# Kernel tuning notes

Measured on AMD Instinct MI355X. Metric: run time of the kernel, lower is better.

Reference implementation:

```python
import jax, jax.numpy as jnp
import numpy as np

N, E, EU, L2, EL, G = 50000, 800000, 400000, 131072, 1048576, 512
ND, ED, H, NH, NL, OUT = 128, 16, 128, 4, 2, 1
HD = H // NH


def _ln(x, g, b):
    m = x.mean(-1, keepdims=True)
    v = ((x - m) ** 2).mean(-1, keepdims=True)
    return (x - m) * jax.lax.rsqrt(v + 1e-5) * g + b


def _gcn(x, w, b, ei, n):
    # GCNConv: add self-loops, symmetric normalization, aggregate at ei[1]
    xw = x @ w.T
    loop = jnp.arange(n)
    src = jnp.concatenate([ei[0], loop])
    dst = jnp.concatenate([ei[1], loop])
    deg = jax.ops.segment_sum(jnp.ones_like(src, x.dtype), dst, n)
    dinv = jnp.where(deg > 0, jax.lax.rsqrt(deg), 0.0)
    norm = (dinv[src] * dinv[dst])[:, None]
    return jax.ops.segment_sum(norm * xw[src], dst, n) + b


def _mha(xs, in_w, in_b, out_w, out_b):
    B, S, _ = xs.shape
    qkv = xs @ in_w.T + in_b                       # [B,S,3H]
    q, k, v = jnp.split(qkv, 3, axis=-1)
    hd = lambda a: a.reshape(B, S, NH, HD).transpose(0, 2, 1, 3)
    q, k, v = hd(q), hd(k), hd(v)
    att = jax.nn.softmax(jnp.einsum('bhqd,bhkd->bhqk', q, k) / jnp.sqrt(jnp.float32(HD)), axis=-1)
    o = jnp.einsum('bhqk,bhkd->bhqd', att, v).transpose(0, 2, 1, 3).reshape(B, S, H)
    return o @ out_w.T + out_b


def _encoder(xs, p):
    # torch TransformerEncoderLayer, post-norm, relu activation, dropout=0 (eval)
    for i in range(NL):
        a = _mha(xs, p['in_w'][i], p['in_b'][i], p['out_w'][i], p['out_b'][i])
        xs = _ln(xs + a, p['ln1_g'][i], p['ln1_b'][i])
        ff = jax.nn.relu(xs @ p['ff1_w'][i].T + p['ff1_b'][i]) @ p['ff2_w'][i].T + p['ff2_b'][i]
        xs = _ln(xs + ff, p['ln2_g'][i], p['ln2_b'][i])
    return xs


def _multi_pool(x, idx, g):
    cnt = jax.ops.segment_sum(jnp.ones((x.shape[0],), x.dtype), idx, g)
    mean = jax.ops.segment_sum(x, idx, g) / jnp.maximum(cnt, 1.0)[:, None]
    mx = jax.ops.segment_max(x, idx, g)
    mn = jax.ops.segment_min(x, idx, g)
    mx = jnp.where(jnp.isfinite(mx), mx, 0.0)
    mn = jnp.where(jnp.isfinite(mn), mn, 0.0)
    return jnp.concatenate([mn, mx, mean], axis=-1)


def setup_inputs() -> dict:
    key = jax.random.key(0)
    ks = jax.random.split(key, 40)
    r = lambda i, shape: jax.random.normal(ks[i], shape, jnp.float32) * 0.02
    inp = {}
    inp['x'] = jax.random.normal(ks[0], (N, ND), jnp.float32)
    inp['edge_attr'] = jax.random.normal(ks[1], (EU, ED), jnp.float32)
    inp['edge_index'] = jax.random.randint(ks[2], (2, E), 0, N)
    inp['unique_edges'] = jax.random.randint(ks[3], (2, EU), 0, N)
    inp['batch'] = jnp.sort(jax.random.randint(ks[4], (N,), 0, G))
    inp['l2_node_mapping'] = jax.random.randint(ks[5], (2, L2), 0, EU)
    inp['l2_edge_index'] = jax.random.randint(ks[6], (2, EL), 0, L2)
    inp['num_graphs'] = G
    inp['lin_edge_w'] = r(7, (H, ED)); inp['lin_edge_b'] = jnp.zeros((H,))
    inp['gcn1_w'] = r(8, (H, ND)); inp['gcn1_b'] = jnp.zeros((H,))
    inp['gcn2_w'] = r(9, (H, H)); inp['gcn2_b'] = jnp.zeros((H,))
    inp['t_in_w'] = r(10, (NL, 3 * H, H)); inp['t_in_b'] = jnp.zeros((NL, 3 * H))
    inp['t_out_w'] = r(11, (NL, H, H)); inp['t_out_b'] = jnp.zeros((NL, H))
    inp['t_ln1_g'] = jnp.ones((NL, H)); inp['t_ln1_b'] = jnp.zeros((NL, H))
    inp['t_ln2_g'] = jnp.ones((NL, H)); inp['t_ln2_b'] = jnp.zeros((NL, H))
    inp['t_ff1_w'] = r(12, (NL, 2 * H, H)); inp['t_ff1_b'] = jnp.zeros((NL, 2 * H))
    inp['t_ff2_w'] = r(13, (NL, H, 2 * H)); inp['t_ff2_b'] = jnp.zeros((NL, H))
    inp['f0_w'] = r(14, (H, 9 * H)); inp['f0_b'] = jnp.zeros((H,))
    inp['f0_g'] = jnp.ones((H,)); inp['f0_beta'] = jnp.zeros((H,))
    inp['f1_w'] = r(15, (H, H)); inp['f1_b'] = jnp.zeros((H,))
    inp['f1_g'] = jnp.ones((H,)); inp['f1_beta'] = jnp.zeros((H,))
    inp['fo_w'] = r(16, (OUT, H)); inp['fo_b'] = jnp.zeros((OUT,))
    return inp


def reference(x, edge_attr, lin_edge_w, lin_edge_b, gcn1_w, gcn1_b, gcn2_w, gcn2_b,
              t_in_w, t_in_b, t_out_w, t_out_b, t_ln1_g, t_ln1_b, t_ln2_g, t_ln2_b,
              t_ff1_w, t_ff1_b, t_ff2_w, t_ff2_b, f0_w, f0_b, f0_g, f0_beta,
              f1_w, f1_b, f1_g, f1_beta, fo_w, fo_b,
              edge_index, unique_edges, batch, l2_node_mapping, l2_edge_index, num_graphs):
    H0_edge = edge_attr @ lin_edge_w.T + lin_edge_b                 # [EU,H]
    H0 = _gcn(x, gcn1_w, gcn1_b, edge_index, x.shape[0])            # [N,H]
    e_idx, f_idx = l2_node_mapping[0], l2_node_mapping[1]
    u, v = unique_edges[0, e_idx], unique_edges[1, e_idx]
    s, t = unique_edges[0, f_idx], unique_edges[1, f_idx]
    H0_set = jnp.stack([H0[u], H0[v], H0[s], H0[t], H0_edge[e_idx], H0_edge[f_idx]], axis=1)  # [L2,6,H]
    tp = dict(in_w=t_in_w, in_b=t_in_b, out_w=t_out_w, out_b=t_out_b,
              ln1_g=t_ln1_g, ln1_b=t_ln1_b, ln2_g=t_ln2_g, ln2_b=t_ln2_b,
              ff1_w=t_ff1_w, ff1_b=t_ff1_b, ff2_w=t_ff2_w, ff2_b=t_ff2_b)
    H1 = _encoder(H0_set, tp).mean(axis=1)                          # [L2,H]
    l2_batch = batch[u]
    H2 = jax.nn.relu(_gcn(H1, gcn2_w, gcn2_b, l2_edge_index, H1.shape[0]))
    H0_pool = _multi_pool(H0, batch, num_graphs)
    H1_pool = _multi_pool(H1, l2_batch, num_graphs)
    H2_pool = _multi_pool(H2, l2_batch, num_graphs)
    Hp = jnp.concatenate([H0_pool, H1_pool, H2_pool], axis=1)       # [G,9H]
    h = jax.nn.gelu(_ln(Hp @ f0_w.T + f0_b, f0_g, f0_beta), approximate=False)
    h = jax.nn.gelu(_ln(h @ f1_w.T + f1_b, f1_g, f1_beta), approximate=False)
    return h @ fo_w.T + fo_b
```

## Files before the change

### kernel.cpp

```cpp
#include <hip/hip_runtime.h>

constexpr int cN  = 50000;
constexpr int cE  = 800000;
constexpr int cEU = 400000;
constexpr int cL2 = 131072;
constexpr int cEL = 1048576;
constexpr int cG  = 512;
constexpr int cH  = 128;
constexpr int cNH = 4;
constexpr int cNL = 2;

constexpr int CAP1 = 64;
constexpr int CAP2 = 48;

constexpr int ESETS = 8;
constexpr int ERT   = ESETS * 6;
constexpr int MT    = 3;
constexpr int QS    = 388;
constexpr int AS    = 264;

constexpr int OFF_QKV = 0;
constexpr int OFF_AH  = 74496;
constexpr int OFF_AL  = OFF_AH + 25344;
constexpr int OFF_ATT = OFF_AL + 25344;
constexpr int OFF_IDX = OFF_ATT + 4608;
constexpr int SMEM_SZ = OFF_IDX + 192;

typedef __attribute__((ext_vector_type(8))) short short8v;
typedef __attribute__((ext_vector_type(4))) float f32x4;

#define DEVI __device__ __forceinline__

DEVI unsigned fmap(float x) {
  unsigned u = __float_as_uint(x);
  return (u & 0x80000000u) ? ~u : (u | 0x80000000u);
}
DEVI float funmap(unsigned m) {
  return __uint_as_float((m & 0x80000000u) ? (m & 0x7FFFFFFFu) : ~m);
}
DEVI float gelu_exact(float x) {
  return 0.5f * x * (1.0f + erff(x * 0.70710678118654752f));
}
DEVI unsigned short f2b_rn(float x) {
  unsigned u = __float_as_uint(x);
  return (unsigned short)((u + 0x7FFFu + ((u >> 16) & 1u)) >> 16);
}
DEVI float b2f(unsigned short h) { return __uint_as_float(((unsigned)h) << 16); }
DEVI void sp2(unsigned short* hi, unsigned short* lo, int idx, float a0, float a1) {
  unsigned short h0 = f2b_rn(a0), h1 = f2b_rn(a1);
  unsigned short l0 = f2b_rn(a0 - b2f(h0)), l1 = f2b_rn(a1 - b2f(h1));
  *(unsigned*)&hi[idx] = (unsigned)h0 | ((unsigned)h1 << 16);
  *(unsigned*)&lo[idx] = (unsigned)l0 | ((unsigned)l1 << 16);
}
DEVI void sp4(unsigned short* hi, unsigned short* lo, int idx, float4 v) {
  unsigned short h0 = f2b_rn(v.x), h1 = f2b_rn(v.y), h2 = f2b_rn(v.z), h3 = f2b_rn(v.w);
  unsigned short l0 = f2b_rn(v.x - b2f(h0)), l1 = f2b_rn(v.y - b2f(h1));
  unsigned short l2 = f2b_rn(v.z - b2f(h2)), l3 = f2b_rn(v.w - b2f(h3));
  uint2 H, L;
  H.x = (unsigned)h0 | ((unsigned)h1 << 16);
  H.y = (unsigned)h2 | ((unsigned)h3 << 16);
  L.x = (unsigned)l0 | ((unsigned)l1 << 16);
  L.y = (unsigned)l2 | ((unsigned)l3 << 16);
  *(uint2*)&hi[idx] = H;
  *(uint2*)&lo[idx] = L;
}

__global__ void fill_k(float* p, float v, int n) {
  int i = blockIdx.x * 256 + threadIdx.x;
  if (i < n) p[i] = v;
}

__global__ void deg_count_k(const int* __restrict__ ei, float* deg, int nE) {
  int e = blockIdx.x * 256 + threadIdx.x;
  if (e < nE) atomicAdd(&deg[ei[nE + e]], 1.0f);
}

__global__ void to_dinv_k(float* deg, int n) {
  int i = blockIdx.x * 256 + threadIdx.x;
  if (i < n) deg[i] = rsqrtf(deg[i]);
}

__global__ void csr_fill_k(const int* __restrict__ ei, int* __restrict__ cnt,
                           int* __restrict__ csr, int cap, int nE) {
  int e = blockIdx.x * 256 + threadIdx.x;
  if (e >= nE) return;
  int s = ei[e], d = ei[nE + e];
  int slot = atomicAdd(&cnt[d], 1);
  if (slot < cap) csr[(long)d * cap + slot] = s;
}

__global__ void split_w_k(const float* __restrict__ src, unsigned short* __restrict__ hi,
                          unsigned short* __restrict__ lo, int n) {
  int i = blockIdx.x * 256 + threadIdx.x;
  if (i < n) {
    float x = src[i];
    unsigned short h = f2b_rn(x);
    hi[i] = h;
    lo[i] = f2b_rn(x - b2f(h));
  }
}

__global__ __launch_bounds__(256) void gemm128_k(const float* __restrict__ A,
                                                 const float* __restrict__ W,
                                                 float* __restrict__ C, int M) {
  __shared__ float At[16][132];
  int c = threadIdx.x & 127, rr = threadIdx.x >> 7;
  int base = blockIdx.x * 128;
  for (int tile = 0; tile < 8; ++tile) {
    int r0 = base + tile * 16;
    if (r0 >= M) break;
    __syncthreads();
    for (int i = threadIdx.x; i < 16 * 32; i += 256) {
      int r = i >> 5, s4 = (i & 31) * 4;
      if (r0 + r < M) *(float4*)&At[r][s4] = *(const float4*)&A[(long)(r0 + r) * cH + s4];
    }
    __syncthreads();
    float acc[8];
    #pragma unroll
    for (int j = 0; j < 8; ++j) acc[j] = 0.f;
    const float* wr = W + (long)c * cH;
    for (int k = 0; k < cH; k += 4) {
      float4 w4 = *(const float4*)(wr + k);
      #pragma unroll
      for (int j = 0; j < 8; ++j) {
        float4 a4 = *(const float4*)&At[rr * 8 + j][k];
        acc[j] = fmaf(a4.x, w4.x, acc[j]);
        acc[j] = fmaf(a4.y, w4.y, acc[j]);
        acc[j] = fmaf(a4.z, w4.z, acc[j]);
        acc[j] = fmaf(a4.w, w4.w, acc[j]);
      }
    }
    #pragma unroll
    for (int j = 0; j < 8; ++j) {
      int r = r0 + rr * 8 + j;
      if (r < M) C[(long)r * cH + c] = acc[j];
    }
  }
}

template<int STORE>
__global__ __launch_bounds__(256) void gcn_gather_k(
    const float* __restrict__ xw, const float* __restrict__ dinv,
    const int* __restrict__ csr, const int* __restrict__ cnt,
    const float* __restrict__ bias, float* __restrict__ out,
    const int* __restrict__ gidx,
    float* __restrict__ sum, unsigned* __restrict__ mx, unsigned* __restrict__ mn,
    float* __restrict__ ccnt, int n, int cap) {
  int wv = threadIdx.x >> 6, lane = threadIdx.x & 63;
  int r = blockIdx.x * 4 + wv;
  if (r >= n) return;
  int c = lane * 2;
  float di = dinv[r];
  float2 v0 = *(const float2*)&xw[(long)r * cH + c];
  float2 b2 = *(const float2*)&bias[c];
  float a0 = b2.x + di * di * v0.x;
  float a1 = b2.y + di * di * v0.y;
  int deg = cnt[r];
  if (deg > cap) deg = cap;
  long base = (long)r * cap;
  for (int k = 0; k < deg; ++k) {
    int s = csr[base + k];
    float w = dinv[s] * di;
    float2 v = *(const float2*)&xw[(long)s * cH + c];
    a0 = fmaf(w, v.x, a0);
    a1 = fmaf(w, v.y, a1);
  }
  if (STORE) {
    float2 o; o.x = a0; o.y = a1;
    *(float2*)&out[(long)r * cH + c] = o;
  } else {
    a0 = fmaxf(a0, 0.f);
    a1 = fmaxf(a1, 0.f);
    int g = gidx[r];
    long b = (long)g * cH + c;
    atomicAdd(&sum[b + 0], a0); atomicAdd(&sum[b + 1], a1);
    atomicMax(&mx[b + 0], fmap(a0)); atomicMax(&mx[b + 1], fmap(a1));
    atomicMin(&mn[b + 0], fmap(a0)); atomicMin(&mn[b + 1], fmap(a1));
    if (lane == 0) atomicAdd(&ccnt[g], 1.0f);
  }
}

__global__ __launch_bounds__(512, 1) void encoder_k(
    const float* __restrict__ H0, const float* __restrict__ EA,
    const float* __restrict__ LEW, const float* __restrict__ LEB,
    const int* __restrict__ ue, const int* __restrict__ l2nm,
    const int* __restrict__ batch,
    const unsigned short* __restrict__ WinH, const unsigned short* __restrict__ WinL,
    const float* __restrict__ Bin,
    const unsigned short* __restrict__ WoutH, const unsigned short* __restrict__ WoutL,
    const float* __restrict__ Bout,
    const float* __restrict__ Ln1g, const float* __restrict__ Ln1b,
    const float* __restrict__ Ln2g, const float* __restrict__ Ln2b,
    const unsigned short* __restrict__ Wf1H, const unsigned short* __restrict__ Wf1L,
    const float* __restrict__ Bf1,
    const unsigned short* __restrict__ Wf2H, const unsigned short* __restrict__ Wf2L,
    const float* __restrict__ Bf2,
    float* __restrict__ H1,
    float* __restrict__ sum1, unsigned* __restrict__ mx1, unsigned* __restrict__ mn1,
    float* __restrict__ cnt1, int* __restrict__ l2b) {
  extern __shared__ char smem[];
  float* QKV = (float*)(smem + OFF_QKV);
  unsigned short* Ahs = (unsigned short*)(smem + OFF_AH);
  unsigned short* Als = (unsigned short*)(smem + OFF_AL);
  float* att = (float*)(smem + OFF_ATT);
  int* nidx = (int*)(smem + OFF_IDX);
  int* eidx = nidx + 32;

  const int tid = threadIdx.x;
  const int lane = tid & 63, wv = tid >> 6;
  const int lr = lane & 15, lq = lane >> 4;
  const int base = blockIdx.x * ESETS;

  if (tid < ESETS) {
    int e = l2nm[base + tid];
    int f = l2nm[cL2 + base + tid];
    eidx[tid * 2 + 0] = e;
    eidx[tid * 2 + 1] = f;
    nidx[tid * 4 + 0] = ue[e];
    nidx[tid * 4 + 1] = ue[cEU + e];
    nidx[tid * 4 + 2] = ue[f];
    nidx[tid * 4 + 3] = ue[cEU + f];
  }
  __syncthreads();
  for (int i = tid; i < 32 * 32; i += 512) {
    int q = i >> 5, s4 = (i & 31) * 4;
    int r = (q >> 2) * 6 + (q & 3);
    float4 v = *(const float4*)&H0[(long)nidx[q] * cH + s4];
    sp4(Ahs, Als, r * AS + s4, v);
  }
  for (int i = tid; i < ESETS * cH; i += 512) {
    int c = (i & 63) * 2, q = i >> 6;
    const float* row = EA + (long)eidx[q] * 16;
    const float* w0 = LEW + c * 16;
    const float* w1 = LEW + (c + 1) * 16;
    float2 bb2 = *(const float2*)&LEB[c];
    float a0 = bb2.x, a1 = bb2.y;
    #pragma unroll
    for (int d = 0; d < 16; ++d) {
      float rv = row[d];
      a0 = fmaf(rv, w0[d], a0);
      a1 = fmaf(rv, w1[d], a1);
    }
    int r = (q >> 1) * 6 + 4 + (q & 1);
    sp2(Ahs, Als, r * AS + c, a0, a1);
  }
  __syncthreads();

  for (int l = 0; l < cNL; ++l) {
    {
      const unsigned short* WH = WinH + (long)l * 384 * 128;
      const unsigned short* WL = WinL + (long)l * 384 * 128;
      const float* BB = Bin + l * 384;
      #pragma unroll
      for (int ni = 0; ni < 3; ++ni) {
        int col = (wv + 8 * ni) * 16 + lr;
        const unsigned short* wp = WH + (long)col * 128 + (lq << 3);
        const unsigned short* wq = WL + (long)col * 128 + (lq << 3);
        f32x4 accH[MT], accL1[MT], accL2[MT];
        #pragma unroll
        for (int m = 0; m < MT; ++m) {
          accH[m] = (f32x4){0.f, 0.f, 0.f, 0.f};
          accL1[m] = (f32x4){0.f, 0.f, 0.f, 0.f};
          accL2[m] = (f32x4){0.f, 0.f, 0.f, 0.f};
        }
        #pragma unroll
        for (int ks = 0; ks < 4; ++ks) {
          short8v bh = *(const short8v*)&wp[ks * 32];
          short8v bl = *(const short8v*)&wq[ks * 32];
          #pragma unroll
          for (int m = 0; m < MT; ++m) {
            int ao = (m * 16 + lr) * AS + (lq << 3) + ks * 32;
            short8v ah = *(const short8v*)&Ahs[ao];
            short8v al = *(const short8v*)&Als[ao];
            accL1[m] = __builtin_amdgcn_mfma_f32_16x16x32_bf16(al, bh, accL1[m], 0, 0, 0);
            accL2[m] = __builtin_amdgcn_mfma_f32_16x16x32_bf16(ah, bl, accL2[m], 0, 0, 0);
            accH[m] = __builtin_amdgcn_mfma_f32_16x16x32_bf16(ah, bh, accH[m], 0, 0, 0);
          }
        }
        float bv = BB[col];
        #pragma unroll
        for (int m = 0; m < MT; ++m) {
          int r0 = m * 16 + (lq << 2);
          #pragma unroll
          for (int j = 0; j < 4; ++j)
            QKV[(r0 + j) * QS + col] = accH[m][j] + (accL1[m][j] + accL2[m][j]) + bv;
        }
      }
    }
    __syncthreads();
    {
      const int s = wv;
      float* attS = att + s * 144;
      if (lane < 24) {
        int h = lane / 6, qt = lane % 6;
        const float* qp = &QKV[(s * 6 + qt) * QS + h * 32];
        float4 qv[8];
        #pragma unroll
        for (int j4 = 0; j4 < 8; ++j4) qv[j4] = *(const float4*)&qp[j4 * 4];
        float sc[6];
        #pragma unroll
        for (int kt = 0; kt < 6; ++kt) {
          const float* kp = &QKV[(s * 6 + kt) * QS + 128 + h * 32];
          float d = 0.f;
          #pragma unroll
          for (int j4 = 0; j4 < 8; ++j4) {
            float4 b4 = *(const float4*)&kp[j4 * 4];
            d = fmaf(qv[j4].x, b4.x, d); d = fmaf(qv[j4].y, b4.y, d);
            d = fmaf(qv[j4].z, b4.z, d); d = fmaf(qv[j4].w, b4.w, d);
          }
          sc[kt] = d * 0.17677669529663687f;
        }
        float mx = sc[0];
        #pragma unroll
        for (int kt = 1; kt < 6; ++kt) mx = fmaxf(mx, sc[kt]);
        float ev[6]; float sum = 0.f;
        #pragma unroll
        for (int kt = 0; kt < 6; ++kt) { ev[kt] = expf(sc[kt] - mx); sum += ev[kt]; }
        float inv = 1.f / sum;
        #pragma unroll
        for (int kt = 0; kt < 6; ++kt) attS[(h * 6 + qt) * 6 + kt] = ev[kt] * inv;
      }
      asm volatile("s_waitcnt lgkmcnt(0)" ::: "memory");
      __builtin_amdgcn_sched_barrier(0);
      {
        int c = lane * 2;
        int h = c >> 5;
        #pragma unroll
        for (int r = 0; r < 6; ++r) {
          const float* arow = &attS[(h * 6 + r) * 6];
          float d0 = 0.f, d1 = 0.f;
          #pragma unroll
          for (int kt = 0; kt < 6; ++kt) {
            float2 v2 = *(const float2*)&QKV[(s * 6 + kt) * QS + 256 + c];
            float a = arow[kt];
            d0 = fmaf(a, v2.x, d0);
            d1 = fmaf(a, v2.y, d1);
          }
          sp2(Ahs, Als, (s * 6 + r) * AS + 128 + c, d0, d1);
        }
      }
    }
    __syncthreads();
    {
      const unsigned short* WH = WoutH + (long)l * 128 * 128;
      const unsigned short* WL = WoutL + (long)l * 128 * 128;
      int col = wv * 16 + lr;
      const unsigned short* wp = WH + (long)col * 128 + (lq << 3);
      const unsigned short* wq = WL + (long)col * 128 + (lq << 3);
      f32x4 accH[MT], accL1[MT], accL2[MT];
      #pragma unroll
      for (int m = 0; m < MT; ++m) {
        accH[m] = (f32x4){0.f, 0.f, 0.f, 0.f};
        accL1[m] = (f32x4){0.f, 0.f, 0.f, 0.f};
        accL2[m] = (f32x4){0.f, 0.f, 0.f, 0.f};
      }
      #pragma unroll
      for (int ks = 0; ks < 4; ++ks) {
        short8v bh = *(const short8v*)&wp[ks * 32];
        short8v bl = *(const short8v*)&wq[ks * 32];
        #pragma unroll
        for (int m = 0; m < MT; ++m) {
          int ao = (m * 16 + lr) * AS + 128 + (lq << 3) + ks * 32;
          short8v ah = *(const short8v*)&Ahs[ao];
          short8v al = *(const short8v*)&Als[ao];
          accL1[m] = __builtin_amdgcn_mfma_f32_16x16x32_bf16(al, bh, accL1[m], 0, 0, 0);
          accL2[m] = __builtin_amdgcn_mfma_f32_16x16x32_bf16(ah, bl, accL2[m], 0, 0, 0);
          accH[m] = __builtin_amdgcn_mfma_f32_16x16x32_bf16(ah, bh, accH[m], 0, 0, 0);
        }
      }
      float bv = Bout[l * 128 + col];
      #pragma unroll
      for (int m = 0; m < MT; ++m) {
        int r0 = m * 16 + (lq << 2);
        #pragma unroll
        for (int j = 0; j < 4; ++j)
          QKV[(r0 + j) * QS + col] = accH[m][j] + (accL1[m][j] + accL2[m][j]) + bv;
      }
    }
    __syncthreads();
    {
      const float* gg = Ln1g + l * cH;
      const float* bb = Ln1b + l * cH;
      #pragma unroll
      for (int p = 0; p < MT; ++p) {
        int r = p * 16 + (tid >> 5);
        int c0 = (tid & 31) * 4;
        ushort4 ah4 = *(const ushort4*)&Ahs[r * AS + c0];
        ushort4 al4 = *(const ushort4*)&Als[r * AS + c0];
        float4 q4 = *(const float4*)&QKV[r * QS + c0];
        float y[4];
        y[0] = b2f(ah4.x) + b2f(al4.x) + q4.x;
        y[1] = b2f(ah4.y) + b2f(al4.y) + q4.y;
        y[2] = b2f(ah4.z) + b2f(al4.z) + q4.z;
        y[3] = b2f(ah4.w) + b2f(al4.w) + q4.w;
        float s = 0.f, s2 = 0.f;
        #pragma unroll
        for (int j = 0; j < 4; ++j) { s += y[j]; s2 += y[j] * y[j]; }
        #pragma unroll
        for (int m = 1; m < 32; m <<= 1) { s += __shfl_xor(s, m, 32); s2 += __shfl_xor(s2, m, 32); }
        float mean = s * (1.f / 128.f);
        float rstd = rsqrtf(s2 * (1.f / 128.f) - mean * mean + 1e-5f);
        float4 g4 = *(const float4*)&gg[c0];
        float4 b4v = *(const float4*)&bb[c0];
        float4 xn4;
        xn4.x = (y[0] - mean) * rstd * g4.x + b4v.x;
        xn4.y = (y[1] - mean) * rstd * g4.y + b4v.y;
        xn4.z = (y[2] - mean) * rstd * g4.z + b4v.z;
        xn4.w = (y[3] - mean) * rstd * g4.w + b4v.w;
        *(float4*)&QKV[r * QS + 128 + c0] = xn4;
        sp4(Ahs, Als, r * AS + c0, xn4);
      }
    }
    __syncthreads();
    {
      const unsigned short* WH = Wf1H + (long)l * 256 * 128;
      const unsigned short* WL = Wf1L + (long)l * 256 * 128;
      #pragma unroll
      for (int ni = 0; ni < 2; ++ni) {
        int col = (wv + 8 * ni) * 16 + lr;
        const unsigned short* wp = WH + (long)col * 128 + (lq << 3);
        const unsigned short* wq = WL + (long)col * 128 + (lq << 3);
        f32x4 accH[MT], accL1[MT], accL2[MT];
        #pragma unroll
        for (int m = 0; m < MT; ++m) {
          accH[m] = (f32x4){0.f, 0.f, 0.f, 0.f};
          accL1[m] = (f32x4){0.f, 0.f, 0.f, 0.f};
          accL2[m] = (f32x4){0.f, 0.f, 0.f, 0.f};
        }
        #pragma unroll
        for (int ks = 0; ks < 4; ++ks) {
          short8v bh = *(const short8v*)&wp[ks * 32];
          short8v bl = *(const short8v*)&wq[ks * 32];
          #pragma unroll
          for (int m = 0; m < MT; ++m) {
            int ao = (m * 16 + lr) * AS + (lq << 3) + ks * 32;
            short8v ah = *(const short8v*)&Ahs[ao];
            short8v al = *(const short8v*)&Als[ao];
            accL1[m] = __builtin_amdgcn_mfma_f32_16x16x32_bf16(al, bh, accL1[m], 0, 0, 0);
            accL2[m] = __builtin_amdgcn_mfma_f32_16x16x32_bf16(ah, bl, accL2[m], 0, 0, 0);
            accH[m] = __builtin_amdgcn_mfma_f32_16x16x32_bf16(ah, bh, accH[m], 0, 0, 0);
          }
        }
        int lc = col + (col >= 128 ? 128 : 0);
        #pragma unroll
        for (int m = 0; m < MT; ++m) {
          int r0 = m * 16 + (lq << 2);
          #pragma unroll
          for (int j = 0; j < 4; ++j)
            QKV[(r0 + j) * QS + lc] = accH[m][j] + (accL1[m][j] + accL2[m][j]);
        }
      }
    }
    __syncthreads();
    for (int i = tid; i < ERT * 128; i += 512) {
      int r = i >> 7, n = (i & 127) * 2;
      int lc = n + (n >= 128 ? 128 : 0);
      float2 v2 = *(const float2*)&QKV[r * QS + lc];
      float2 bb2 = *(const float2*)&Bf1[l * 256 + n];
      float h0 = fmaxf(v2.x + bb2.x, 0.f);
      float h1 = fmaxf(v2.y + bb2.y, 0.f);
      sp2(Ahs, Als, r * AS + n, h0, h1);
    }
    __syncthreads();
    {
      const unsigned short* WH = Wf2H + (long)l * 128 * 256;
      const unsigned short* WL = Wf2L + (long)l * 128 * 256;
      int col = wv * 16 + lr;
      const unsigned short* wp = WH + (long)col * 256 + (lq << 3);
      const unsigned short* wq = WL + (long)col * 256 + (lq << 3);
      f32x4 accH[MT], accL1[MT], accL2[MT];
      #pragma unroll
      for (int m = 0; m < MT; ++m) {
        accH[m] = (f32x4){0.f, 0.f, 0.f, 0.f};
        accL1[m] = (f32x4){0.f, 0.f, 0.f, 0.f};
        accL2[m] = (f32x4){0.f, 0.f, 0.f, 0.f};
      }
      #pragma unroll
      for (int ks = 0; ks < 8; ++ks) {
        short8v bh = *(const short8v*)&wp[ks * 32];
        short8v bl = *(const short8v*)&wq[ks * 32];
        #pragma unroll
        for (int m = 0; m < MT; ++m) {
          int ao = (m * 16 + lr) * AS + (lq << 3) + ks * 32;
          short8v ah = *(const short8v*)&Ahs[ao];
          short8v al = *(const short8v*)&Als[ao];
          accL1[m] = __builtin_amdgcn_mfma_f32_16x16x32_bf16(al, bh, accL1[m], 0, 0, 0);
          accL2[m] = __builtin_amdgcn_mfma_f32_16x16x32_bf16(ah, bl, accL2[m], 0, 0, 0);
          accH[m] = __builtin_amdgcn_mfma_f32_16x16x32_bf16(ah, bh, accH[m], 0, 0, 0);
        }
      }
      float bv = Bf2[l * 128 + col];
      #pragma unroll
      for (int m = 0; m < MT; ++m) {
        int r0 = m * 16 + (lq << 2);
        #pragma unroll
        for (int j = 0; j < 4; ++j)
          QKV[(r0 + j) * QS + col] = accH[m][j] + (accL1[m][j] + accL2[m][j]) + bv;
      }
    }
    __syncthreads();
    {
      const float* gg = Ln2g + l * cH;
      const float* bb = Ln2b + l * cH;
      #pragma unroll
      for (int p = 0; p < MT; ++p) {
        int r = p * 16 + (tid >> 5);
        int c0 = (tid & 31) * 4;
        float4 qa = *(const float4*)&QKV[r * QS + 128 + c0];
        float4 qb = *(const float4*)&QKV[r * QS + c0];
        float y[4];
        y[0] = qa.x + qb.x; y[1] = qa.y + qb.y;
        y[2] = qa.z + qb.z; y[3] = qa.w + qb.w;
        float s = 0.f, s2 = 0.f;
        #pragma unroll
        for (int j = 0; j < 4; ++j) { s += y[j]; s2 += y[j] * y[j]; }
        #pragma unroll
        for (int m = 1; m < 32; m <<= 1) { s += __shfl_xor(s, m, 32); s2 += __shfl_xor(s2, m, 32); }
        float mean = s * (1.f / 128.f);
        float rstd = rsqrtf(s2 * (1.f / 128.f) - mean * mean + 1e-5f);
        float4 g4 = *(const float4*)&gg[c0];
        float4 b4v = *(const float4*)&bb[c0];
        float4 xn4;
        xn4.x = (y[0] - mean) * rstd * g4.x + b4v.x;
        xn4.y = (y[1] - mean) * rstd * g4.y + b4v.y;
        xn4.z = (y[2] - mean) * rstd * g4.z + b4v.z;
        xn4.w = (y[3] - mean) * rstd * g4.w + b4v.w;
        sp4(Ahs, Als, r * AS + c0, xn4);
      }
    }
    __syncthreads();
  }

  {
    int s = tid >> 6, c = (tid & 63) * 2;
    float m0 = 0.f, m1 = 0.f;
    #pragma unroll
    for (int t = 0; t < 6; ++t) {
      unsigned hh = *(const unsigned*)&Ahs[(s * 6 + t) * AS + c];
      unsigned ll = *(const unsigned*)&Als[(s * 6 + t) * AS + c];
      m0 += b2f((unsigned short)(hh & 0xFFFFu)) + b2f((unsigned short)(ll & 0xFFFFu));
      m1 += b2f((unsigned short)(hh >> 16)) + b2f((unsigned short)(ll >> 16));
    }
    float v0 = m0 * (1.f / 6.f), v1 = m1 * (1.f / 6.f);
    float2 o; o.x = v0; o.y = v1;
    *(float2*)&H1[(long)(base + s) * cH + c] = o;
    int g = batch[nidx[s * 4]];
    long b = (long)g * cH + c;
    atomicAdd(&sum1[b + 0], v0);  atomicAdd(&sum1[b + 1], v1);
    atomicMax(&mx1[b + 0], fmap(v0)); atomicMax(&mx1[b + 1], fmap(v1));
    atomicMin(&mn1[b + 0], fmap(v0)); atomicMin(&mn1[b + 1], fmap(v1));
    if (c == 0) {
      atomicAdd(&cnt1[g], 1.0f);
      l2b[base + s] = g;
    }
  }
}

__global__ void init_stats3_k(char* ST, size_t stride) {
  int i = blockIdx.x * 256 + threadIdx.x;
  if (i >= cG * cH) return;
  #pragma unroll
  for (int p = 0; p < 3; ++p) {
    char* b = ST + (size_t)p * stride;
    ((float*)b)[i] = 0.f;
    ((unsigned*)(b + (size_t)cG * cH * 4))[i] = 0u;
    ((unsigned*)(b + (size_t)cG * cH * 8))[i] = 0xFFFFFFFFu;
    if (i < cG) ((float*)(b + (size_t)cG * cH * 12))[i] = 0.f;
  }
}

__global__ void pool_sorted_k(const float* __restrict__ X, const int* __restrict__ gidx,
                              float* sum, unsigned* mx, unsigned* mn, float* cnt, int n) {
  long t = (long)blockIdx.x * 256 + threadIdx.x;
  int q = (int)(t & 31) * 4;
  long r0 = (t >> 5) * 8;
  if (r0 >= n) return;
  int gcur = -1;
  float s0 = 0, s1 = 0, s2 = 0, s3 = 0, cc = 0;
  float x0 = 0, x1 = 0, x2 = 0, x3 = 0;
  float n0 = 0, n1 = 0, n2 = 0, n3 = 0;
  for (int k = 0; k < 8; ++k) {
    long r = r0 + k;
    if (r >= n) break;
    int g = gidx[r];
    float4 v = *(const float4*)&X[r * cH + q];
    if (g != gcur) {
      if (gcur >= 0) {
        long b = (long)gcur * cH + q;
        atomicAdd(&sum[b + 0], s0); atomicAdd(&sum[b + 1], s1);
        atomicAdd(&sum[b + 2], s2); atomicAdd(&sum[b + 3], s3);
        atomicMax(&mx[b + 0], fmap(x0)); atomicMax(&mx[b + 1], fmap(x1));
        atomicMax(&mx[b + 2], fmap(x2)); atomicMax(&mx[b + 3], fmap(x3));
        atomicMin(&mn[b + 0], fmap(n0)); atomicMin(&mn[b + 1], fmap(n1));
        atomicMin(&mn[b + 2], fmap(n2)); atomicMin(&mn[b + 3], fmap(n3));
        if (q == 0) atomicAdd(&cnt[gcur], cc);
      }
      gcur = g;
      s0 = v.x; s1 = v.y; s2 = v.z; s3 = v.w;
      x0 = v.x; x1 = v.y; x2 = v.z; x3 = v.w;
      n0 = v.x; n1 = v.y; n2 = v.z; n3 = v.w;
      cc = 1.f;
    } else {
      s0 += v.x; s1 += v.y; s2 += v.z; s3 += v.w;
      x0 = fmaxf(x0, v.x); x1 = fmaxf(x1, v.y); x2 = fmaxf(x2, v.z); x3 = fmaxf(x3, v.w);
      n0 = fminf(n0, v.x); n1 = fminf(n1, v.y); n2 = fminf(n2, v.z); n3 = fminf(n3, v.w);
      cc += 1.f;
    }
  }
  if (gcur >= 0) {
    long b = (long)gcur * cH + q;
    atomicAdd(&sum[b + 0], s0); atomicAdd(&sum[b + 1], s1);
    atomicAdd(&sum[b + 2], s2); atomicAdd(&sum[b + 3], s3);
    atomicMax(&mx[b + 0], fmap(x0)); atomicMax(&mx[b + 1], fmap(x1));
    atomicMax(&mx[b + 2], fmap(x2)); atomicMax(&mx[b + 3], fmap(x3));
    atomicMin(&mn[b + 0], fmap(n0)); atomicMin(&mn[b + 1], fmap(n1));
    atomicMin(&mn[b + 2], fmap(n2)); atomicMin(&mn[b + 3], fmap(n3));
    if (q == 0) atomicAdd(&cnt[gcur], cc);
  }
}

__global__ __launch_bounds__(128) void mlp_k(
    const char* __restrict__ ST, size_t stride,
    const float* __restrict__ f0w, const float* __restrict__ f0b,
    const float* __restrict__ f0g, const float* __restrict__ f0bb,
    const float* __restrict__ f1w, const float* __restrict__ f1b,
    const float* __restrict__ f1g, const float* __restrict__ f1bb,
    const float* __restrict__ fow, const float* __restrict__ fob,
    float* __restrict__ out) {
  __shared__ float hin[1152];
  __shared__ float red[8];
  int g = blockIdx.x, tid = threadIdx.x;
  #pragma unroll
  for (int p = 0; p < 3; ++p) {
    const char* b = ST + (size_t)p * stride;
    const float* sum = (const float*)b;
    const unsigned* mx = (const unsigned*)(b + (size_t)cG * cH * 4);
    const unsigned* mn = (const unsigned*)(b + (size_t)cG * cH * 8);
    const float* cnt = (const float*)(b + (size_t)cG * cH * 12);
    int idx = g * cH + tid;
    float ct = cnt[g];
    float mean = sum[idx] / fmaxf(ct, 1.f);
    float mxv = (ct > 0.f) ? funmap(mx[idx]) : 0.f;
    float mnv = (ct > 0.f) ? funmap(mn[idx]) : 0.f;
    hin[p * 384 + tid] = mnv;
    hin[p * 384 + 128 + tid] = mxv;
    hin[p * 384 + 256 + tid] = mean;
  }
  __syncthreads();
  float acc = f0b[tid];
  {
    const float* wr = f0w + (long)tid * 1152;
    for (int k = 0; k < 1152; k += 4) {
      float4 w4 = *(const float4*)(wr + k);
      float4 h4 = *(const float4*)&hin[k];
      acc = fmaf(h4.x, w4.x, acc);
      acc = fmaf(h4.y, w4.y, acc);
      acc = fmaf(h4.z, w4.z, acc);
      acc = fmaf(h4.w, w4.w, acc);
    }
  }
  float s = acc, s2 = acc * acc;
  #pragma unroll
  for (int m = 1; m < 64; m <<= 1) { s += __shfl_xor(s, m); s2 += __shfl_xor(s2, m); }
  if ((tid & 63) == 0) { red[tid >> 6] = s; red[4 + (tid >> 6)] = s2; }
  __syncthreads();
  s = red[0] + red[1]; s2 = red[4] + red[5];
  {
    float mean = s * (1.f / 128.f);
    float rstd = rsqrtf(s2 * (1.f / 128.f) - mean * mean + 1e-5f);
    float xn = (acc - mean) * rstd * f0g[tid] + f0bb[tid];
    float h0 = gelu_exact(xn);
    __syncthreads();
    hin[tid] = h0;
  }
  __syncthreads();
  acc = f1b[tid];
  {
    const float* wr = f1w + (long)tid * 128;
    for (int k = 0; k < 128; k += 4) {
      float4 w4 = *(const float4*)(wr + k);
      float4 h4 = *(const float4*)&hin[k];
      acc = fmaf(h4.x, w4.x, acc);
      acc = fmaf(h4.y, w4.y, acc);
      acc = fmaf(h4.z, w4.z, acc);
      acc = fmaf(h4.w, w4.w, acc);
    }
  }
  s = acc; s2 = acc * acc;
  #pragma unroll
  for (int m = 1; m < 64; m <<= 1) { s += __shfl_xor(s, m); s2 += __shfl_xor(s2, m); }
  __syncthreads();
  if ((tid & 63) == 0) { red[tid >> 6] = s; red[4 + (tid >> 6)] = s2; }
  __syncthreads();
  s = red[0] + red[1]; s2 = red[4] + red[5];
  float h1;
  {
    float mean = s * (1.f / 128.f);
    float rstd = rsqrtf(s2 * (1.f / 128.f) - mean * mean + 1e-5f);
    float xn = (acc - mean) * rstd * f1g[tid] + f1bb[tid];
    h1 = gelu_exact(xn);
  }
  float p = h1 * fow[tid];
  #pragma unroll
  for (int m = 1; m < 64; m <<= 1) p += __shfl_xor(p, m);
  __syncthreads();
  if ((tid & 63) == 0) red[tid >> 6] = p;
  __syncthreads();
  if (tid == 0) out[g] = red[0] + red[1] + fob[0];
}

extern "C" void kernel_launch(void* const* d_in, const int* in_sizes, int n_in,
                              void* d_out, int out_size, void* d_ws, size_t ws_size,
                              hipStream_t stream) {
  const float* x     = (const float*)d_in[0];
  const float* ea    = (const float*)d_in[1];
  const int*   ei    = (const int*)d_in[2];
  const int*   ue    = (const int*)d_in[3];
  const int*   batch = (const int*)d_in[4];
  const int*   l2nm  = (const int*)d_in[5];
  const int*   l2ei  = (const int*)d_in[6];
  const float* lew   = (const float*)d_in[8];
  const float* leb   = (const float*)d_in[9];
  const float* g1w   = (const float*)d_in[10];
  const float* g1b   = (const float*)d_in[11];
  const float* g2w   = (const float*)d_in[12];
  const float* g2b   = (const float*)d_in[13];
  const float* tinw  = (const float*)d_in[14];
  const float* tinb  = (const float*)d_in[15];
  const float* toutw = (const float*)d_in[16];
  const float* toutb = (const float*)d_in[17];
  const float* tl1g  = (const float*)d_in[18];
  const float* tl1b  = (const float*)d_in[19];
  const float* tl2g  = (const float*)d_in[20];
  const float* tl2b  = (const float*)d_in[21];
  const float* tf1w  = (const float*)d_in[22];
  const float* tf1b  = (const float*)d_in[23];
  const float* tf2w  = (const float*)d_in[24];
  const float* tf2b  = (const float*)d_in[25];
  const float* f0w   = (const float*)d_in[26];
  const float* f0b   = (const float*)d_in[27];
  const float* f0g   = (const float*)d_in[28];
  const float* f0bb  = (const float*)d_in[29];
  const float* f1w   = (const float*)d_in[30];
  const float* f1b   = (const float*)d_in[31];
  const float* f1g   = (const float*)d_in[32];
  const float* f1bb  = (const float*)d_in[33];
  const float* fow   = (const float*)d_in[34];
  const float* fob   = (const float*)d_in[35];
  float* out = (float*)d_out;

  char* ws = (char*)d_ws;
  size_t off = 0;
  float* H1  = (float*)(ws + off);  off += (size_t)cL2 * cH * 4;
  float* H0  = (float*)(ws + off);  off += (size_t)cL2 * cH * 4;
  float* XW  = (float*)(ws + off);  off += (size_t)cL2 * cH * 4;
  float* DEG = (float*)(ws + off);  off += (size_t)cL2 * 4;
  int*   L2B = (int*)(ws + off);    off += (size_t)cL2 * 4;
  int*   CNT = (int*)(ws + off);    off += (size_t)cL2 * 4;
  char*  ST  = ws + off;            off += 3 * ((size_t)cG * cH * 4 * 3 + cG * 4);
  int*   CSR1 = (int*)(ws + off);   off += (size_t)cN * CAP1 * 4;
  int*   CSR2 = (int*)(ws + off);   off += (size_t)cL2 * CAP2 * 4;
  unsigned short* WinH  = (unsigned short*)(ws + off); off += (size_t)cNL * 384 * 128 * 2;
  unsigned short* WinL  = (unsigned short*)(ws + off); off += (size_t)cNL * 384 * 128 * 2;
  unsigned short* WoutH = (unsigned short*)(ws + off); off += (size_t)cNL * 128 * 128 * 2;
  unsigned short* WoutL = (unsigned short*)(ws + off); off += (size_t)cNL * 128 * 128 * 2;
  unsigned short* Wf1H  = (unsigned short*)(ws + off); off += (size_t)cNL * 256 * 128 * 2;
  unsigned short* Wf1L  = (unsigned short*)(ws + off); off += (size_t)cNL * 256 * 128 * 2;
  unsigned short* Wf2H  = (unsigned short*)(ws + off); off += (size_t)cNL * 128 * 256 * 2;
  unsigned short* Wf2L  = (unsigned short*)(ws + off); off += (size_t)cNL * 128 * 256 * 2;

  size_t st_stride = (size_t)cG * cH * 4 * 3 + cG * 4;
  auto stat = [&](int p) {
    char* b = ST + p * st_stride;
    struct S { float* sum; unsigned* mx; unsigned* mn; float* cnt; } s;
    s.sum = (float*)b;
    s.mx  = (unsigned*)(b + (size_t)cG * cH * 4);
    s.mn  = (unsigned*)(b + (size_t)cG * cH * 8);
    s.cnt = (float*)(b + (size_t)cG * cH * 12);
    return s;
  };
  auto s0 = stat(0), s1 = stat(1), s2 = stat(2);

  split_w_k<<<(cNL * 384 * 128 + 255) / 256, 256, 0, stream>>>(tinw, WinH, WinL, cNL * 384 * 128);
  split_w_k<<<(cNL * 128 * 128 + 255) / 256, 256, 0, stream>>>(toutw, WoutH, WoutL, cNL * 128 * 128);
  split_w_k<<<(cNL * 256 * 128 + 255) / 256, 256, 0, stream>>>(tf1w, Wf1H, Wf1L, cNL * 256 * 128);
  split_w_k<<<(cNL * 128 * 256 + 255) / 256, 256, 0, stream>>>(tf2w, Wf2H, Wf2L, cNL * 128 * 256);
  init_stats3_k<<<(cG * cH + 255) / 256, 256, 0, stream>>>(ST, st_stride);

  gemm128_k<<<(cN + 127) / 128, 256, 0, stream>>>(x, g1w, XW, cN);
  fill_k<<<(cN + 255) / 256, 256, 0, stream>>>(DEG, 1.0f, cN);
  deg_count_k<<<(cE + 255) / 256, 256, 0, stream>>>(ei, DEG, cE);
  to_dinv_k<<<(cN + 255) / 256, 256, 0, stream>>>(DEG, cN);
  fill_k<<<(cN + 255) / 256, 256, 0, stream>>>((float*)CNT, 0.0f, cN);
  csr_fill_k<<<(cE + 255) / 256, 256, 0, stream>>>(ei, CNT, CSR1, CAP1, cE);
  gcn_gather_k<1><<<(cN + 3) / 4, 256, 0, stream>>>(XW, DEG, CSR1, CNT, g1b, H0,
      nullptr, nullptr, nullptr, nullptr, nullptr, cN, CAP1);

  hipFuncSetAttribute(reinterpret_cast<const void*>(encoder_k),
                      hipFuncAttributeMaxDynamicSharedMemorySize, 131072);
  encoder_k<<<cL2 / ESETS, 512, SMEM_SZ, stream>>>(H0, ea, lew, leb, ue, l2nm, batch,
      WinH, WinL, tinb, WoutH, WoutL, toutb, tl1g, tl1b, tl2g, tl2b,
      Wf1H, Wf1L, tf1b, Wf2H, Wf2L, tf2b, H1,
      s1.sum, s1.mx, s1.mn, s1.cnt, L2B);

  pool_sorted_k<<<(int)((((long)(cN + 7) / 8) * 32 + 255) / 256), 256, 0, stream>>>(
      H0, batch, s0.sum, s0.mx, s0.mn, s0.cnt, cN);

  gemm128_k<<<(cL2 + 127) / 128, 256, 0, stream>>>(H1, g2w, XW, cL2);
  fill_k<<<(cL2 + 255) / 256, 256, 0, stream>>>(DEG, 1.0f, cL2);
  deg_count_k<<<(cEL + 255) / 256, 256, 0, stream>>>(l2ei, DEG, cEL);
  to_dinv_k<<<(cL2 + 255) / 256, 256, 0, stream>>>(DEG, cL2);
  fill_k<<<(cL2 + 255) / 256, 256, 0, stream>>>((float*)CNT, 0.0f, cL2);
  csr_fill_k<<<(cEL + 255) / 256, 256, 0, stream>>>(l2ei, CNT, CSR2, CAP2, cEL);
  gcn_gather_k<0><<<(cL2 + 3) / 4, 256, 0, stream>>>(XW, DEG, CSR2, CNT, g2b, nullptr,
      L2B, s2.sum, s2.mx, s2.mn, s2.cnt, cL2, CAP2);

  mlp_k<<<cG, 128, 0, stream>>>(ST, st_stride, f0w, f0b, f0g, f0bb, f1w, f1b, f1g, f1bb, fow, fob, out);
}
```

Before: 4.360 ms.

## Shrink encoder tile to four sets for multi-block occupancy; derive degree from CSR counts

The encoder kernel now processes 4 edge-sets per block instead of 8, shrinking shared memory to about 73KB and raising launch bounds so several blocks can share a CU. The MFMA tile count drops to 2 with padded rows zeroed and guarded stores. The separate degree atomic pass is removed and inverse sqrt degree is computed from the CSR fill counts. The trade-off is more blocks with padding waste (24 of 32 rows used) and lower weight reuse per block. It also relies on the CSR counts being uncapped atomic counts.

```diff
diff --git a/kernel.cpp b/kernel.cpp
--- a/kernel.cpp
+++ b/kernel.cpp
@@ -13,18 +13,18 @@
 constexpr int CAP1 = 64;
 constexpr int CAP2 = 48;
 
-constexpr int ESETS = 8;
+constexpr int ESETS = 4;
 constexpr int ERT   = ESETS * 6;
-constexpr int MT    = 3;
+constexpr int MT    = 2;
 constexpr int QS    = 388;
 constexpr int AS    = 264;
 
 constexpr int OFF_QKV = 0;
-constexpr int OFF_AH  = 74496;
-constexpr int OFF_AL  = OFF_AH + 25344;
-constexpr int OFF_ATT = OFF_AL + 25344;
-constexpr int OFF_IDX = OFF_ATT + 4608;
-constexpr int SMEM_SZ = OFF_IDX + 192;
+constexpr int OFF_AH  = 37248;
+constexpr int OFF_AL  = OFF_AH + 16896;
+constexpr int OFF_ATT = OFF_AL + 16896;
+constexpr int OFF_IDX = OFF_ATT + 2304;
+constexpr int SMEM_SZ = OFF_IDX + 96;
 
 typedef __attribute__((ext_vector_type(8))) short short8v;
 typedef __attribute__((ext_vector_type(4))) float f32x4;
@@ -70,14 +70,9 @@
   if (i < n) p[i] = v;
 }
 
-__global__ void deg_count_k(const int* __restrict__ ei, float* deg, int nE) {
-  int e = blockIdx.x * 256 + threadIdx.x;
-  if (e < nE) atomicAdd(&deg[ei[nE + e]], 1.0f);
-}
-
-__global__ void to_dinv_k(float* deg, int n) {
+__global__ void cnt_to_dinv_k(const int* __restrict__ cnt, float* __restrict__ dinv, int n) {
   int i = blockIdx.x * 256 + threadIdx.x;
-  if (i < n) deg[i] = rsqrtf(deg[i]);
+  if (i < n) dinv[i] = rsqrtf((float)cnt[i] + 1.0f);
 }
 
 __global__ void csr_fill_k(const int* __restrict__ ei, int* __restrict__ cnt,
@@ -180,7 +175,7 @@
   }
 }
 
-__global__ __launch_bounds__(512, 1) void encoder_k(
+__global__ __launch_bounds__(512, 4) void encoder_k(
     const float* __restrict__ H0, const float* __restrict__ EA,
     const float* __restrict__ LEW, const float* __restrict__ LEB,
     const int* __restrict__ ue, const int* __restrict__ l2nm,
@@ -204,7 +199,7 @@
   unsigned short* Als = (unsigned short*)(smem + OFF_AL);
   float* att = (float*)(smem + OFF_ATT);
   int* nidx = (int*)(smem + OFF_IDX);
-  int* eidx = nidx + 32;
+  int* eidx = nidx + 16;
 
   const int tid = threadIdx.x;
   const int lane = tid & 63, wv = tid >> 6;
@@ -222,13 +217,19 @@
     nidx[tid * 4 + 3] = ue[cEU + f];
   }
   __syncthreads();
-  for (int i = tid; i < 32 * 32; i += 512) {
+  for (int i = tid; i < (32 - ERT) * AS; i += 512) {
+    Ahs[ERT * AS + i] = 0;
+    Als[ERT * AS + i] = 0;
+  }
+  {
+    int i = tid;
     int q = i >> 5, s4 = (i & 31) * 4;
     int r = (q >> 2) * 6 + (q & 3);
     float4 v = *(const float4*)&H0[(long)nidx[q] * cH + s4];
     sp4(Ahs, Als, r * AS + s4, v);
   }
-  for (int i = tid; i < ESETS * cH; i += 512) {
+  {
+    int i = tid;
     int c = (i & 63) * 2, q = i >> 6;
     const float* row = EA + (long)eidx[q] * 16;
     const float* w0 = LEW + c * 16;
@@ -281,14 +282,16 @@
         #pragma unroll
         for (int m = 0; m < MT; ++m) {
           int r0 = m * 16 + (lq << 2);
-          #pragma unroll
-          for (int j = 0; j < 4; ++j)
-            QKV[(r0 + j) * QS + col] = accH[m][j] + (accL1[m][j] + accL2[m][j]) + bv;
-        }
-      }
-    }
-    __syncthreads();
-    {
+          if (r0 < ERT) {
+            #pragma unroll
+            for (int j = 0; j < 4; ++j)
+              QKV[(r0 + j) * QS + col] = accH[m][j] + (accL1[m][j] + accL2[m][j]) + bv;
+          }
+        }
+      }
+    }
+    __syncthreads();
+    if (wv < ESETS) {
       const int s = wv;
       float* attS = att + s * 144;
       if (lane < 24) {
@@ -372,9 +375,11 @@
       #pragma unroll
       for (int m = 0; m < MT; ++m) {
         int r0 = m * 16 + (lq << 2);
-        #pragma unroll
-        for (int j = 0; j < 4; ++j)
-          QKV[(r0 + j) * QS + col] = accH[m][j] + (accL1[m][j] + accL2[m][j]) + bv;
+        if (r0 < ERT) {
+          #pragma unroll
+          for (int j = 0; j < 4; ++j)
+            QKV[(r0 + j) * QS + col] = accH[m][j] + (accL1[m][j] + accL2[m][j]) + bv;
+        }
       }
     }
     __syncthreads();
@@ -382,33 +387,35 @@
       const float* gg = Ln1g + l * cH;
       const float* bb = Ln1b + l * cH;
       #pragma unroll
-      for (int p = 0; p < MT; ++p) {
+      for (int p = 0; p < 2; ++p) {
         int r = p * 16 + (tid >> 5);
-        int c0 = (tid & 31) * 4;
-        ushort4 ah4 = *(const ushort4*)&Ahs[r * AS + c0];
-        ushort4 al4 = *(const ushort4*)&Als[r * AS + c0];
-        float4 q4 = *(const float4*)&QKV[r * QS + c0];
-        float y[4];
-        y[0] = b2f(ah4.x) + b2f(al4.x) + q4.x;
-        y[1] = b2f(ah4.y) + b2f(al4.y) + q4.y;
-        y[2] = b2f(ah4.z) + b2f(al4.z) + q4.z;
-        y[3] = b2f(ah4.w) + b2f(al4.w) + q4.w;
-        float s = 0.f, s2 = 0.f;
-        #pragma unroll
-        for (int j = 0; j < 4; ++j) { s += y[j]; s2 += y[j] * y[j]; }
-        #pragma unroll
-        for (int m = 1; m < 32; m <<= 1) { s += __shfl_xor(s, m, 32); s2 += __shfl_xor(s2, m, 32); }
-        float mean = s * (1.f / 128.f);
-        float rstd = rsqrtf(s2 * (1.f / 128.f) - mean * mean + 1e-5f);
-        float4 g4 = *(const float4*)&gg[c0];
-        float4 b4v = *(const float4*)&bb[c0];
-        float4 xn4;
-        xn4.x = (y[0] - mean) * rstd * g4.x + b4v.x;
-        xn4.y = (y[1] - mean) * rstd * g4.y + b4v.y;
-        xn4.z = (y[2] - mean) * rstd * g4.z + b4v.z;
-        xn4.w = (y[3] - mean) * rstd * g4.w + b4v.w;
-        *(float4*)&QKV[r * QS + 128 + c0] = xn4;
-        sp4(Ahs, Als, r * AS + c0, xn4);
+        if (r < ERT) {
+          int c0 = (tid & 31) * 4;
+          ushort4 ah4 = *(const ushort4*)&Ahs[r * AS + c0];
+          ushort4 al4 = *(const ushort4*)&Als[r * AS + c0];
+          float4 q4 = *(const float4*)&QKV[r * QS + c0];
+          float y[4];
+          y[0] = b2f(ah4.x) + b2f(al4.x) + q4.x;
+          y[1] = b2f(ah4.y) + b2f(al4.y) + q4.y;
+          y[2] = b2f(ah4.z) + b2f(al4.z) + q4.z;
+          y[3] = b2f(ah4.w) + b2f(al4.w) + q4.w;
+          float s = 0.f, s2 = 0.f;
+          #pragma unroll
+          for (int j = 0; j < 4; ++j) { s += y[j]; s2 += y[j] * y[j]; }
+          #pragma unroll
+          for (int m = 1; m < 32; m <<= 1) { s += __shfl_xor(s, m, 32); s2 += __shfl_xor(s2, m, 32); }
+          float mean = s * (1.f / 128.f);
+          float rstd = rsqrtf(s2 * (1.f / 128.f) - mean * mean + 1e-5f);
+          float4 g4 = *(const float4*)&gg[c0];
+          float4 b4v = *(const float4*)&bb[c0];
+          float4 xn4;
+          xn4.x = (y[0] - mean) * rstd * g4.x + b4v.x;
+          xn4.y = (y[1] - mean) * rstd * g4.y + b4v.y;
+          xn4.z = (y[2] - mean) * rstd * g4.z + b4v.z;
+          xn4.w = (y[3] - mean) * rstd * g4.w + b4v.w;
+          *(float4*)&QKV[r * QS + 128 + c0] = xn4;
+          sp4(Ahs, Als, r * AS + c0, xn4);
+        }
       }
     }
     __syncthreads();
@@ -445,9 +452,11 @@
         #pragma unroll
         for (int m = 0; m < MT; ++m) {
           int r0 = m * 16 + (lq << 2);
-          #pragma unroll
-          for (int j = 0; j < 4; ++j)
-            QKV[(r0 + j) * QS + lc] = accH[m][j] + (accL1[m][j] + accL2[m][j]);
+          if (r0 < ERT) {
+            #pragma unroll
+            for (int j = 0; j < 4; ++j)
+              QKV[(r0 + j) * QS + lc] = accH[m][j] + (accL1[m][j] + accL2[m][j]);
+          }
         }
       }
     }
@@ -493,9 +502,11 @@
       #pragma unroll
       for (int m = 0; m < MT; ++m) {
         int r0 = m * 16 + (lq << 2);
-        #pragma unroll
-        for (int j = 0; j < 4; ++j)
-          QKV[(r0 + j) * QS + col] = accH[m][j] + (accL1[m][j] + accL2[m][j]) + bv;
+        if (r0 < ERT) {
+          #pragma unroll
+          for (int j = 0; j < 4; ++j)
+            QKV[(r0 + j) * QS + col] = accH[m][j] + (accL1[m][j] + accL2[m][j]) + bv;
+        }
       }
     }
     __syncthreads();
@@ -503,35 +514,37 @@
       const float* gg = Ln2g + l * cH;
       const float* bb = Ln2b + l * cH;
       #pragma unroll
-      for (int p = 0; p < MT; ++p) {
+      for (int p = 0; p < 2; ++p) {
         int r = p * 16 + (tid >> 5);
-        int c0 = (tid & 31) * 4;
-        float4 qa = *(const float4*)&QKV[r * QS + 128 + c0];
-        float4 qb = *(const float4*)&QKV[r * QS + c0];
-        float y[4];
-        y[0] = qa.x + qb.x; y[1] = qa.y + qb.y;
-        y[2] = qa.z + qb.z; y[3] = qa.w + qb.w;
-        float s = 0.f, s2 = 0.f;
-        #pragma unroll
-        for (int j = 0; j < 4; ++j) { s += y[j]; s2 += y[j] * y[j]; }
-        #pragma unroll
-        for (int m = 1; m < 32; m <<= 1) { s += __shfl_xor(s, m, 32); s2 += __shfl_xor(s2, m, 32); }
-        float mean = s * (1.f / 128.f);
-        float rstd = rsqrtf(s2 * (1.f / 128.f) - mean * mean + 1e-5f);
-        float4 g4 = *(const float4*)&gg[c0];
-        float4 b4v = *(const float4*)&bb[c0];
-        float4 xn4;
-        xn4.x = (y[0] - mean) * rstd * g4.x + b4v.x;
-        xn4.y = (y[1] - mean) * rstd * g4.y + b4v.y;
-        xn4.z = (y[2] - mean) * rstd * g4.z + b4v.z;
-        xn4.w = (y[3] - mean) * rstd * g4.w + b4v.w;
-        sp4(Ahs, Als, r * AS + c0, xn4);
-      }
-    }
-    __syncthreads();
-  }
-
-  {
+        if (r < ERT) {
+          int c0 = (tid & 31) * 4;
+          float4 qa = *(const float4*)&QKV[r * QS + 128 + c0];
+          float4 qb = *(const float4*)&QKV[r * QS + c0];
+          float y[4];
+          y[0] = qa.x + qb.x; y[1] = qa.y + qb.y;
+          y[2] = qa.z + qb.z; y[3] = qa.w + qb.w;
+          float s = 0.f, s2 = 0.f;
+          #pragma unroll
+          for (int j = 0; j < 4; ++j) { s += y[j]; s2 += y[j] * y[j]; }
+          #pragma unroll
+          for (int m = 1; m < 32; m <<= 1) { s += __shfl_xor(s, m, 32); s2 += __shfl_xor(s2, m, 32); }
+          float mean = s * (1.f / 128.f);
+          float rstd = rsqrtf(s2 * (1.f / 128.f) - mean * mean + 1e-5f);
+          float4 g4 = *(const float4*)&gg[c0];
+          float4 b4v = *(const float4*)&bb[c0];
+          float4 xn4;
+          xn4.x = (y[0] - mean) * rstd * g4.x + b4v.x;
+          xn4.y = (y[1] - mean) * rstd * g4.y + b4v.y;
+          xn4.z = (y[2] - mean) * rstd * g4.z + b4v.z;
+          xn4.w = (y[3] - mean) * rstd * g4.w + b4v.w;
+          sp4(Ahs, Als, r * AS + c0, xn4);
+        }
+      }
+    }
+    __syncthreads();
+  }
+
+  if (tid < ESETS * 64) {
     int s = tid >> 6, c = (tid & 63) * 2;
     float m0 = 0.f, m1 = 0.f;
     #pragma unroll
@@ -788,11 +801,9 @@
   init_stats3_k<<<(cG * cH + 255) / 256, 256, 0, stream>>>(ST, st_stride);
 
   gemm128_k<<<(cN + 127) / 128, 256, 0, stream>>>(x, g1w, XW, cN);
-  fill_k<<<(cN + 255) / 256, 256, 0, stream>>>(DEG, 1.0f, cN);
-  deg_count_k<<<(cE + 255) / 256, 256, 0, stream>>>(ei, DEG, cE);
-  to_dinv_k<<<(cN + 255) / 256, 256, 0, stream>>>(DEG, cN);
   fill_k<<<(cN + 255) / 256, 256, 0, stream>>>((float*)CNT, 0.0f, cN);
   csr_fill_k<<<(cE + 255) / 256, 256, 0, stream>>>(ei, CNT, CSR1, CAP1, cE);
+  cnt_to_dinv_k<<<(cN + 255) / 256, 256, 0, stream>>>(CNT, DEG, cN);
   gcn_gather_k<1><<<(cN + 3) / 4, 256, 0, stream>>>(XW, DEG, CSR1, CNT, g1b, H0,
       nullptr, nullptr, nullptr, nullptr, nullptr, cN, CAP1);
 
@@ -807,11 +818,9 @@
       H0, batch, s0.sum, s0.mx, s0.mn, s0.cnt, cN);
 
   gemm128_k<<<(cL2 + 127) / 128, 256, 0, stream>>>(H1, g2w, XW, cL2);
-  fill_k<<<(cL2 + 255) / 256, 256, 0, stream>>>(DEG, 1.0f, cL2);
-  deg_count_k<<<(cEL + 255) / 256, 256, 0, stream>>>(l2ei, DEG, cEL);
-  to_dinv_k<<<(cL2 + 255) / 256, 256, 0, stream>>>(DEG, cL2);
   fill_k<<<(cL2 + 255) / 256, 256, 0, stream>>>((float*)CNT, 0.0f, cL2);
   csr_fill_k<<<(cEL + 255) / 256, 256, 0, stream>>>(l2ei, CNT, CSR2, CAP2, cEL);
+  cnt_to_dinv_k<<<(cL2 + 255) / 256, 256, 0, stream>>>(CNT, DEG, cL2);
   gcn_gather_k<0><<<(cL2 + 3) / 4, 256, 0, stream>>>(XW, DEG, CSR2, CNT, g2b, nullptr,
       L2B, s2.sum, s2.mx, s2.mn, s2.cnt, cL2, CAP2);
 
```

Result: slower. 6.594 ms (+51.2%).
